# Kernel tuning notes

Hardware: AMD Instinct MI355X
Metric: run time of the kernel (lower is better)

Reference implementation:

```python
import jax, jax.numpy as jnp
import numpy as np

B, S, E, H = 8, 2048, 384, 6
D = E // H  # head dim = 64


def setup_inputs() -> dict:
    key = jax.random.key(0)
    ks = jax.random.split(key, 5)
    s = 1.0 / np.sqrt(E)
    return {
        "x": jax.random.normal(ks[0], (B, S, E), dtype=jnp.float32),
        "Wq": jax.random.normal(ks[1], (E, E), dtype=jnp.float32) * s,
        "Wk": jax.random.normal(ks[2], (E, E), dtype=jnp.float32) * s,
        "Wv": jax.random.normal(ks[3], (E, E), dtype=jnp.float32) * s,
        "Wo": jax.random.normal(ks[4], (E, E), dtype=jnp.float32) * s,
        "bo": jnp.zeros((E,), dtype=jnp.float32),
    }


def reference(x, Wq, Wk, Wv, Wo, bo):
    b, s, e = x.shape
    # QKV projections (torch Linear with bias=False: x @ W.T; here W stored as [in,out])
    q = (x @ Wq).reshape(b, s, H, D).transpose(0, 2, 1, 3)  # [b,h,s,d]
    k = (x @ Wk).reshape(b, s, H, D).transpose(0, 2, 1, 3)
    v = (x @ Wv).reshape(b, s, H, D).transpose(0, 2, 1, 3)
    scores = jnp.einsum("bhqd,bhkd->bhqk", q, k) / jnp.sqrt(jnp.asarray(D, x.dtype))
    causal = jnp.tril(jnp.ones((s, s), dtype=bool))
    scores = jnp.where(causal, scores, -jnp.inf)
    attn = jax.nn.softmax(scores, axis=-1)
    # NOTE: original applies dropout but then uses the PRE-dropout softmax for @V,
    # so dropout is a no-op; we faithfully omit it.
    out = jnp.einsum("bhqk,bhkd->bhqd", attn, v)  # [b,h,s,d]
    out = out.transpose(0, 2, 1, 3).reshape(b, s, e)
    return out @ Wo + bo
```

## Files before the change

kernel.cpp:

```cpp
#include <hip/hip_runtime.h>
#include <hip/hip_bf16.h>
#include <cstdint>
#include <cstddef>

typedef __attribute__((ext_vector_type(8))) short short8;
typedef __attribute__((ext_vector_type(4))) float f32x4;

#define S_LEN 2048
#define EMB 384
#define NH 6
#define HD 64
#define NB 8
#define QSCALE 0.180336880f

__device__ __forceinline__ unsigned short f2bf(float f) {
  unsigned u = __builtin_bit_cast(unsigned, f);
  u += 0x7fffu + ((u >> 16) & 1u);
  return (unsigned short)(u >> 16);
}

__global__ __launch_bounds__(256) void k_prep(
    const float* __restrict__ x, unsigned short* __restrict__ xb,
    const float* __restrict__ Wq, const float* __restrict__ Wk,
    const float* __restrict__ Wv, const float* __restrict__ Wo,
    unsigned short* __restrict__ Wqt, unsigned short* __restrict__ Wkt,
    unsigned short* __restrict__ Wvt, unsigned short* __restrict__ Wot) {
  const int tid = threadIdx.x;
  if (blockIdx.x < 1536) {
    int i = blockIdx.x * 256 + tid;
    const int n4 = (NB * S_LEN * EMB) / 4;
    for (; i < n4; i += 1536 * 256) {
      const float4 v = reinterpret_cast<const float4*>(x)[i];
      ushort4 o;
      o.x = f2bf(v.x); o.y = f2bf(v.y); o.z = f2bf(v.z); o.w = f2bf(v.w);
      reinterpret_cast<ushort4*>(xb)[i] = o;
    }
  } else {
    const int idx = (blockIdx.x - 1536) * 256 + tid;
    const int mat = idx / 147456;
    const int rem = idx - mat * 147456;
    const int k = rem / 384;
    const int n = rem - k * 384;
    const float* W = (mat == 0) ? Wq : (mat == 1) ? Wk : (mat == 2) ? Wv : Wo;
    unsigned short* Wt = (mat == 0) ? Wqt : (mat == 1) ? Wkt : (mat == 2) ? Wvt : Wot;
    Wt[n * 384 + k] = f2bf(W[rem]);
  }
}

__global__ __launch_bounds__(256) void k_qkv(
    const unsigned short* __restrict__ xb,
    const unsigned short* __restrict__ Wqt,
    const unsigned short* __restrict__ Wkt,
    const unsigned short* __restrict__ Wvt,
    unsigned short* __restrict__ Qb,
    unsigned short* __restrict__ Kb,
    unsigned short* __restrict__ Vb) {
  __shared__ __attribute__((aligned(16))) unsigned short La[128 * 72];

  const int tid = threadIdx.x;
  const int lane = tid & 63;
  const int w = tid >> 6;
  const int wr = w >> 1, wc = w & 1;
  const int lr = lane & 15, lg = lane >> 4;
  const int m0 = blockIdx.x * 128;
  const int wsel = blockIdx.y / 3;
  const int n0 = (blockIdx.y % 3) * 128;
  const unsigned short* Wt = (wsel == 0) ? Wqt : (wsel == 1) ? Wkt : Wvt;
  unsigned short* Out = (wsel == 0) ? Qb : (wsel == 1) ? Kb : Vb;

  const int srow = tid >> 3;
  const int sg = tid & 7;

  f32x4 acc[4][4] = {};
  short8 st[4];
#pragma unroll
  for (int i = 0; i < 4; ++i)
    st[i] = *reinterpret_cast<const short8*>(
        xb + (size_t)(m0 + i * 32 + srow) * EMB + sg * 8);

  for (int kt = 0; kt < 6; ++kt) {
    __syncthreads();
#pragma unroll
    for (int i = 0; i < 4; ++i)
      *reinterpret_cast<short8*>(&La[(i * 32 + srow) * 72 + sg * 8]) = st[i];
    __syncthreads();
    if (kt < 5) {
      const int kn = (kt + 1) * 64;
#pragma unroll
      for (int i = 0; i < 4; ++i)
        st[i] = *reinterpret_cast<const short8*>(
            xb + (size_t)(m0 + i * 32 + srow) * EMB + kn + sg * 8);
    }
#pragma unroll
    for (int kk = 0; kk < 2; ++kk) {
      short8 a[4], b[4];
#pragma unroll
      for (int ms = 0; ms < 4; ++ms)
        a[ms] = *reinterpret_cast<const short8*>(
            &La[(wr * 64 + ms * 16 + lr) * 72 + kk * 32 + lg * 8]);
#pragma unroll
      for (int ns = 0; ns < 4; ++ns)
        b[ns] = *reinterpret_cast<const short8*>(
            Wt + (size_t)(n0 + wc * 64 + ns * 16 + lr) * EMB + kt * 64 + kk * 32 + lg * 8);
#pragma unroll
      for (int ms = 0; ms < 4; ++ms)
#pragma unroll
        for (int ns = 0; ns < 4; ++ns)
          acc[ms][ns] = __builtin_amdgcn_mfma_f32_16x16x32_bf16(
              a[ms], b[ns], acc[ms][ns], 0, 0, 0);
    }
  }

  const float sc = (wsel == 0) ? QSCALE : 1.0f;
#pragma unroll
  for (int ms = 0; ms < 4; ++ms)
#pragma unroll
    for (int ns = 0; ns < 4; ++ns)
#pragma unroll
      for (int r = 0; r < 4; ++r) {
        const int m = m0 + wr * 64 + ms * 16 + lg * 4 + r;
        const int n = n0 + wc * 64 + ns * 16 + lr;
        const int bb = m >> 11;
        const int s = m & 2047;
        const int h = n >> 6;
        const int d = n & 63;
        Out[(((size_t)bb * NH + h) * S_LEN + s) * HD + d] = f2bf(acc[ms][ns][r] * sc);
      }
}

__global__ __launch_bounds__(256) void k_vt(const unsigned short* __restrict__ Vb,
                                            unsigned short* __restrict__ Vtg) {
  __shared__ unsigned short L[64 * 65];
  const int tid = threadIdx.x;
  const int g = tid & 7;
  const int h = tid >> 3;
  const int st = blockIdx.x;
  const int bh = blockIdx.y;
  const unsigned short* src = Vb + (size_t)bh * S_LEN * HD + (size_t)st * 64 * HD;
  unsigned short* dst = Vtg + (size_t)bh * S_LEN * HD;

#pragma unroll
  for (int c = 0; c < 2; ++c) {
    const int s = h + 32 * c;
    const short8 v = *reinterpret_cast<const short8*>(src + s * HD + g * 8);
#pragma unroll
    for (int j = 0; j < 8; ++j) L[s * 65 + g * 8 + j] = (unsigned short)v[j];
  }
  __syncthreads();
#pragma unroll
  for (int c = 0; c < 2; ++c) {
    const int d = h + 32 * c;
    short8 v;
#pragma unroll
    for (int j = 0; j < 8; ++j) v[j] = (short)L[(g * 8 + j) * 65 + d];
    *reinterpret_cast<short8*>(dst + (size_t)d * S_LEN + st * 64 + g * 8) = v;
  }
}

__global__ __launch_bounds__(256) void k_attn(
    const unsigned short* __restrict__ Qb,
    const unsigned short* __restrict__ Kb,
    const unsigned short* __restrict__ Vtg,
    unsigned short* __restrict__ Ob) {
  __shared__ __attribute__((aligned(16))) unsigned short Ks[64 * 64];
  __shared__ __attribute__((aligned(16))) unsigned short Vt[64 * 64];
  __shared__ __attribute__((aligned(16))) unsigned short Ps[64 * 64];

  const int tid = threadIdx.x;
  const int lane = tid & 63;
  const int w = tid >> 6;
  const int lr = lane & 15, lg = lane >> 4;

  const int lin = blockIdx.y * 16 + blockIdx.x;
  const int swz = (lin & 7) * 96 + (lin >> 3);
  const int pair = swz & 15;
  const int bh = swz >> 4;

  const unsigned short* Qp = Qb + (size_t)bh * S_LEN * HD;
  const unsigned short* Kp = Kb + (size_t)bh * S_LEN * HD;
  const unsigned short* Vp = Vtg + (size_t)bh * S_LEN * HD;
  const int b = bh / NH, hh = bh - b * NH;

  const int srow = tid >> 3;
  const int sslot = tid & 7;
  const int wsl0 = (sslot ^ (srow & 7)) << 3;

  for (int phase = 0; phase < 2; ++phase) {
    const int qt = phase ? (31 - pair) : pair;
    const int qbase = qt * 64 + w * 16;

    const short8 aq0 = *reinterpret_cast<const short8*>(Qp + (size_t)(qbase + lr) * HD + lg * 8);
    const short8 aq1 = *reinterpret_cast<const short8*>(Qp + (size_t)(qbase + lr) * HD + 32 + lg * 8);

    f32x4 o[4] = {};
    float l_i[4] = {0.f, 0.f, 0.f, 0.f};

    short8 pk0 = *reinterpret_cast<const short8*>(Kp + (size_t)srow * HD + sslot * 8);
    short8 pk1 = *reinterpret_cast<const short8*>(Kp + (size_t)(srow + 32) * HD + sslot * 8);
    short8 pv0 = *reinterpret_cast<const short8*>(Vp + (size_t)srow * S_LEN + sslot * 8);
    short8 pv1 = *reinterpret_cast<const short8*>(Vp + (size_t)(srow + 32) * S_LEN + sslot * 8);

    for (int t = 0; t <= qt; ++t) {
      __syncthreads();
      *reinterpret_cast<short8*>(&Ks[srow * 64 + wsl0]) = pk0;
      *reinterpret_cast<short8*>(&Ks[(srow + 32) * 64 + wsl0]) = pk1;
      *reinterpret_cast<short8*>(&Vt[srow * 64 + wsl0]) = pv0;
      *reinterpret_cast<short8*>(&Vt[(srow + 32) * 64 + wsl0]) = pv1;
      __syncthreads();

      if (t < qt) {
        const int tn = (t + 1) * 64;
        pk0 = *reinterpret_cast<const short8*>(Kp + (size_t)(tn + srow) * HD + sslot * 8);
        pk1 = *reinterpret_cast<const short8*>(Kp + (size_t)(tn + srow + 32) * HD + sslot * 8);
        pv0 = *reinterpret_cast<const short8*>(Vp + (size_t)srow * S_LEN + tn + sslot * 8);
        pv1 = *reinterpret_cast<const short8*>(Vp + (size_t)(srow + 32) * S_LEN + tn + sslot * 8);
      }

      float sv[4][4];
#pragma unroll
      for (int ks = 0; ks < 4; ++ks) {
        const int kstart = t * 64 + ks * 16;
        if (kstart > qbase + 15) {
#pragma unroll
          for (int r = 0; r < 4; ++r) sv[ks][r] = -1e30f;
        } else {
          const int krow = ks * 16 + lr;
          const int kx = krow & 7;
          const short8 bk0 = *reinterpret_cast<const short8*>(&Ks[krow * 64 + ((lg ^ kx) << 3)]);
          const short8 bk1 = *reinterpret_cast<const short8*>(&Ks[krow * 64 + (((4 + lg) ^ kx) << 3)]);
          f32x4 s = {};
          s = __builtin_amdgcn_mfma_f32_16x16x32_bf16(aq0, bk0, s, 0, 0, 0);
          s = __builtin_amdgcn_mfma_f32_16x16x32_bf16(aq1, bk1, s, 0, 0, 0);
          if (kstart + 15 <= qbase) {
#pragma unroll
            for (int r = 0; r < 4; ++r) sv[ks][r] = s[r];
          } else {
            const int kg = kstart + lr;
#pragma unroll
            for (int r = 0; r < 4; ++r)
              sv[ks][r] = (kg <= qbase + lg * 4 + r) ? s[r] : -1e30f;
          }
        }
      }

#pragma unroll
      for (int r = 0; r < 4; ++r) {
        const int q = w * 16 + lg * 4 + r;
        const int qx = q & 7;
        const int abase = q * 64 + (lr & 7);
        const int sp = lr >> 3;
        float p[4];
#pragma unroll
        for (int ks = 0; ks < 4; ++ks) p[ks] = __builtin_amdgcn_exp2f(sv[ks][r]);
        l_i[r] += (p[0] + p[1]) + (p[2] + p[3]);
#pragma unroll
        for (int ks = 0; ks < 4; ++ks)
          Ps[abase + ((((ks << 1) | sp) ^ qx) << 3)] = f2bf(p[ks]);
      }

      const int qrow = w * 16 + lr;
      const int qx2 = qrow & 7;
#pragma unroll
      for (int kk = 0; kk < 2; ++kk) {
        const short8 ap = *reinterpret_cast<const short8*>(
            &Ps[qrow * 64 + (((kk * 4 + lg) ^ qx2) << 3)]);
#pragma unroll
        for (int ns = 0; ns < 4; ++ns) {
          const int vrow = ns * 16 + lr;
          const short8 bv = *reinterpret_cast<const short8*>(
              &Vt[vrow * 64 + (((kk * 4 + lg) ^ (vrow & 7)) << 3)]);
          o[ns] = __builtin_amdgcn_mfma_f32_16x16x32_bf16(ap, bv, o[ns], 0, 0, 0);
        }
      }
    }

#pragma unroll
    for (int r = 0; r < 4; ++r) {
      float l = l_i[r];
      l += __shfl_xor(l, 1);
      l += __shfl_xor(l, 2);
      l += __shfl_xor(l, 4);
      l += __shfl_xor(l, 8);
      l_i[r] = 1.0f / l;
    }
#pragma unroll
    for (int ns = 0; ns < 4; ++ns)
#pragma unroll
      for (int r = 0; r < 4; ++r) {
        const int qg = qbase + lg * 4 + r;
        const float val = o[ns][r] * l_i[r];
        Ob[((size_t)(b * S_LEN + qg)) * EMB + hh * HD + ns * 16 + lr] = f2bf(val);
      }
  }
}

__global__ __launch_bounds__(256) void k_oproj(
    const unsigned short* __restrict__ Ob,
    const unsigned short* __restrict__ Wot,
    const float* __restrict__ bo,
    float* __restrict__ out) {
  __shared__ __attribute__((aligned(16))) unsigned short La[128 * 72];

  const int tid = threadIdx.x;
  const int lane = tid & 63;
  const int w = tid >> 6;
  const int wr = w >> 1, wc = w & 1;
  const int lr = lane & 15, lg = lane >> 4;
  const int m0 = blockIdx.x * 128;
  const int n0 = blockIdx.y * 128;

  const int srow = tid >> 3;
  const int sg = tid & 7;

  f32x4 acc[4][4] = {};
  short8 st[4];
#pragma unroll
  for (int i = 0; i < 4; ++i)
    st[i] = *reinterpret_cast<const short8*>(
        Ob + (size_t)(m0 + i * 32 + srow) * EMB + sg * 8);

  for (int kt = 0; kt < 6; ++kt) {
    __syncthreads();
#pragma unroll
    for (int i = 0; i < 4; ++i)
      *reinterpret_cast<short8*>(&La[(i * 32 + srow) * 72 + sg * 8]) = st[i];
    __syncthreads();
    if (kt < 5) {
      const int kn = (kt + 1) * 64;
#pragma unroll
      for (int i = 0; i < 4; ++i)
        st[i] = *reinterpret_cast<const short8*>(
            Ob + (size_t)(m0 + i * 32 + srow) * EMB + kn + sg * 8);
    }
#pragma unroll
    for (int kk = 0; kk < 2; ++kk) {
      short8 a[4], b[4];
#pragma unroll
      for (int ms = 0; ms < 4; ++ms)
        a[ms] = *reinterpret_cast<const short8*>(
            &La[(wr * 64 + ms * 16 + lr) * 72 + kk * 32 + lg * 8]);
#pragma unroll
      for (int ns = 0; ns < 4; ++ns)
        b[ns] = *reinterpret_cast<const short8*>(
            Wot + (size_t)(n0 + wc * 64 + ns * 16 + lr) * EMB + kt * 64 + kk * 32 + lg * 8);
#pragma unroll
      for (int ms = 0; ms < 4; ++ms)
#pragma unroll
        for (int ns = 0; ns < 4; ++ns)
          acc[ms][ns] = __builtin_amdgcn_mfma_f32_16x16x32_bf16(
              a[ms], b[ns], acc[ms][ns], 0, 0, 0);
    }
  }

#pragma unroll
  for (int ms = 0; ms < 4; ++ms)
#pragma unroll
    for (int ns = 0; ns < 4; ++ns)
#pragma unroll
      for (int r = 0; r < 4; ++r) {
        const int m = m0 + wr * 64 + ms * 16 + lg * 4 + r;
        const int n = n0 + wc * 64 + ns * 16 + lr;
        out[(size_t)m * EMB + n] = acc[ms][ns][r] + bo[n];
      }
}

extern "C" void kernel_launch(void* const* d_in, const int* in_sizes, int n_in,
                              void* d_out, int out_size, void* d_ws, size_t ws_size,
                              hipStream_t stream) {
  const float* x  = (const float*)d_in[0];
  const float* Wq = (const float*)d_in[1];
  const float* Wk = (const float*)d_in[2];
  const float* Wv = (const float*)d_in[3];
  const float* Wo = (const float*)d_in[4];
  const float* bo = (const float*)d_in[5];
  float* out = (float*)d_out;

  uint8_t* ws = (uint8_t*)d_ws;
  unsigned short* xb  = (unsigned short*)(ws);
  unsigned short* Wqt = (unsigned short*)(ws + 12582912);
  unsigned short* Wkt = (unsigned short*)(ws + 12877824);
  unsigned short* Wvt = (unsigned short*)(ws + 13172736);
  unsigned short* Wot = (unsigned short*)(ws + 13467648);
  unsigned short* Qb  = (unsigned short*)(ws + 13762560);
  unsigned short* Kb  = (unsigned short*)(ws + 26345472);
  unsigned short* Vb  = (unsigned short*)(ws + 38928384);
  unsigned short* Ob  = (unsigned short*)(ws + 51511296);
  unsigned short* VT  = xb;

  hipLaunchKernelGGL(k_prep, dim3(3840), dim3(256), 0, stream,
                     x, xb, Wq, Wk, Wv, Wo, Wqt, Wkt, Wvt, Wot);
  hipLaunchKernelGGL(k_qkv, dim3(128, 9), dim3(256), 0, stream,
                     xb, Wqt, Wkt, Wvt, Qb, Kb, Vb);
  hipLaunchKernelGGL(k_vt, dim3(S_LEN / 64, NB * NH), dim3(256), 0, stream, Vb, VT);
  hipLaunchKernelGGL(k_attn, dim3(16, 48), dim3(256), 0, stream, Qb, Kb, VT, Ob);
  hipLaunchKernelGGL(k_oproj, dim3(128, 3), dim3(256), 0, stream, Ob, Wot, bo, out);
}
```

Baseline: 215.5 us.

## Fuse V transpose into QKV GEMM, tile weight transpose, split attention blocks

The V transpose moves into the QKV GEMM epilogue through an LDS swizzled tile, which removes the separate k_vt kernel and a round trip of V through global memory. The weight conversion in prep now uses LDS-tiled transposes instead of scattered scalar writes. Attention now launches one block per query tile, longest tiles first, instead of pairing tiles inside a block, and adds s_setprio around the MFMA sections. The GEMMs register double-buffer the B operand. The changes add code complexity and register pressure.

```diff
diff --git a/kernel.cpp b/kernel.cpp
--- a/kernel.cpp
+++ b/kernel.cpp
@@ -14,9 +14,7 @@
 #define QSCALE 0.180336880f
 
 __device__ __forceinline__ unsigned short f2bf(float f) {
-  unsigned u = __builtin_bit_cast(unsigned, f);
-  u += 0x7fffu + ((u >> 16) & 1u);
-  return (unsigned short)(u >> 16);
+  return __builtin_bit_cast(unsigned short, __float2bfloat16(f));
 }
 
 __global__ __launch_bounds__(256) void k_prep(
@@ -36,14 +34,34 @@
       reinterpret_cast<ushort4*>(xb)[i] = o;
     }
   } else {
-    const int idx = (blockIdx.x - 1536) * 256 + tid;
-    const int mat = idx / 147456;
-    const int rem = idx - mat * 147456;
-    const int k = rem / 384;
-    const int n = rem - k * 384;
+    __shared__ unsigned short Lw[64 * 66];
+    const int bx2 = blockIdx.x - 1536;
+    const int mat = bx2 / 36;
+    const int tile = bx2 - mat * 36;
+    const int k0 = (tile / 6) * 64;
+    const int n0 = (tile % 6) * 64;
     const float* W = (mat == 0) ? Wq : (mat == 1) ? Wk : (mat == 2) ? Wv : Wo;
     unsigned short* Wt = (mat == 0) ? Wqt : (mat == 1) ? Wkt : (mat == 2) ? Wvt : Wot;
-    Wt[n * 384 + k] = f2bf(W[rem]);
+    const int f4 = tid & 15;
+#pragma unroll
+    for (int it = 0; it < 4; ++it) {
+      const int kl = it * 16 + (tid >> 4);
+      const float4 v = reinterpret_cast<const float4*>(W + (size_t)(k0 + kl) * EMB + n0)[f4];
+      Lw[kl * 66 + f4 * 4 + 0] = f2bf(v.x);
+      Lw[kl * 66 + f4 * 4 + 1] = f2bf(v.y);
+      Lw[kl * 66 + f4 * 4 + 2] = f2bf(v.z);
+      Lw[kl * 66 + f4 * 4 + 3] = f2bf(v.w);
+    }
+    __syncthreads();
+    const int g = tid & 7;
+#pragma unroll
+    for (int it = 0; it < 2; ++it) {
+      const int nl = it * 32 + (tid >> 3);
+      short8 o;
+#pragma unroll
+      for (int j = 0; j < 8; ++j) o[j] = (short)Lw[(g * 8 + j) * 66 + nl];
+      *reinterpret_cast<short8*>(Wt + (size_t)(n0 + nl) * EMB + k0 + g * 8) = o;
+    }
   }
 }
 
@@ -54,8 +72,9 @@
     const unsigned short* __restrict__ Wvt,
     unsigned short* __restrict__ Qb,
     unsigned short* __restrict__ Kb,
-    unsigned short* __restrict__ Vb) {
+    unsigned short* __restrict__ Vtb) {
   __shared__ __attribute__((aligned(16))) unsigned short La[128 * 72];
+  __shared__ __attribute__((aligned(16))) unsigned short Lt[64 * 136];
 
   const int tid = threadIdx.x;
   const int lane = tid & 63;
@@ -66,19 +85,28 @@
   const int wsel = blockIdx.y / 3;
   const int n0 = (blockIdx.y % 3) * 128;
   const unsigned short* Wt = (wsel == 0) ? Wqt : (wsel == 1) ? Wkt : Wvt;
-  unsigned short* Out = (wsel == 0) ? Qb : (wsel == 1) ? Kb : Vb;
 
   const int srow = tid >> 3;
   const int sg = tid & 7;
 
   f32x4 acc[4][4] = {};
   short8 st[4];
+  short8 breg[2][2][4];
+
 #pragma unroll
   for (int i = 0; i < 4; ++i)
     st[i] = *reinterpret_cast<const short8*>(
         xb + (size_t)(m0 + i * 32 + srow) * EMB + sg * 8);
-
+#pragma unroll
+  for (int kk = 0; kk < 2; ++kk)
+#pragma unroll
+    for (int ns = 0; ns < 4; ++ns)
+      breg[0][kk][ns] = *reinterpret_cast<const short8*>(
+          Wt + (size_t)(n0 + wc * 64 + ns * 16 + lr) * EMB + kk * 32 + lg * 8);
+
+#pragma unroll
   for (int kt = 0; kt < 6; ++kt) {
+    const int cur = kt & 1, nxt = cur ^ 1;
     __syncthreads();
 #pragma unroll
     for (int i = 0; i < 4; ++i)
@@ -90,70 +118,76 @@
       for (int i = 0; i < 4; ++i)
         st[i] = *reinterpret_cast<const short8*>(
             xb + (size_t)(m0 + i * 32 + srow) * EMB + kn + sg * 8);
+#pragma unroll
+      for (int kk = 0; kk < 2; ++kk)
+#pragma unroll
+        for (int ns = 0; ns < 4; ++ns)
+          breg[nxt][kk][ns] = *reinterpret_cast<const short8*>(
+              Wt + (size_t)(n0 + wc * 64 + ns * 16 + lr) * EMB + kn + kk * 32 + lg * 8);
     }
 #pragma unroll
     for (int kk = 0; kk < 2; ++kk) {
-      short8 a[4], b[4];
+      short8 a[4];
 #pragma unroll
       for (int ms = 0; ms < 4; ++ms)
         a[ms] = *reinterpret_cast<const short8*>(
             &La[(wr * 64 + ms * 16 + lr) * 72 + kk * 32 + lg * 8]);
 #pragma unroll
-      for (int ns = 0; ns < 4; ++ns)
-        b[ns] = *reinterpret_cast<const short8*>(
-            Wt + (size_t)(n0 + wc * 64 + ns * 16 + lr) * EMB + kt * 64 + kk * 32 + lg * 8);
-#pragma unroll
       for (int ms = 0; ms < 4; ++ms)
 #pragma unroll
         for (int ns = 0; ns < 4; ++ns)
           acc[ms][ns] = __builtin_amdgcn_mfma_f32_16x16x32_bf16(
-              a[ms], b[ns], acc[ms][ns], 0, 0, 0);
-    }
-  }
-
-  const float sc = (wsel == 0) ? QSCALE : 1.0f;
-#pragma unroll
-  for (int ms = 0; ms < 4; ++ms)
-#pragma unroll
-    for (int ns = 0; ns < 4; ++ns)
-#pragma unroll
-      for (int r = 0; r < 4; ++r) {
-        const int m = m0 + wr * 64 + ms * 16 + lg * 4 + r;
-        const int n = n0 + wc * 64 + ns * 16 + lr;
-        const int bb = m >> 11;
-        const int s = m & 2047;
-        const int h = n >> 6;
-        const int d = n & 63;
-        Out[(((size_t)bb * NH + h) * S_LEN + s) * HD + d] = f2bf(acc[ms][ns][r] * sc);
+              a[ms], breg[cur][kk][ns], acc[ms][ns], 0, 0, 0);
+    }
+  }
+
+  if (wsel != 2) {
+    unsigned short* Out = (wsel == 0) ? Qb : Kb;
+    const float sc = (wsel == 0) ? QSCALE : 1.0f;
+#pragma unroll
+    for (int ms = 0; ms < 4; ++ms)
+#pragma unroll
+      for (int ns = 0; ns < 4; ++ns)
+#pragma unroll
+        for (int r = 0; r < 4; ++r) {
+          const int m = m0 + wr * 64 + ms * 16 + lg * 4 + r;
+          const int n = n0 + wc * 64 + ns * 16 + lr;
+          const int bb = m >> 11;
+          const int s = m & 2047;
+          const int h = n >> 6;
+          const int d = n & 63;
+          Out[(((size_t)bb * NH + h) * S_LEN + s) * HD + d] = f2bf(acc[ms][ns][r] * sc);
+        }
+  } else {
+    const int bb = m0 >> 11;
+    const int s0 = m0 & 2047;
+#pragma unroll
+    for (int p = 0; p < 2; ++p) {
+      __syncthreads();
+      if (wc == p) {
+#pragma unroll
+        for (int ms = 0; ms < 4; ++ms)
+#pragma unroll
+          for (int ns = 0; ns < 4; ++ns)
+#pragma unroll
+            for (int r = 0; r < 4; ++r) {
+              const int dl = ns * 16 + lr;
+              const int ml = wr * 64 + ms * 16 + lg * 4 + r;
+              Lt[dl * 136 + (((ml >> 3) ^ (dl & 7)) << 3) + (ml & 7)] = f2bf(acc[ms][ns][r]);
+            }
       }
-}
-
-__global__ __launch_bounds__(256) void k_vt(const unsigned short* __restrict__ Vb,
-                                            unsigned short* __restrict__ Vtg) {
-  __shared__ unsigned short L[64 * 65];
-  const int tid = threadIdx.x;
-  const int g = tid & 7;
-  const int h = tid >> 3;
-  const int st = blockIdx.x;
-  const int bh = blockIdx.y;
-  const unsigned short* src = Vb + (size_t)bh * S_LEN * HD + (size_t)st * 64 * HD;
-  unsigned short* dst = Vtg + (size_t)bh * S_LEN * HD;
-
-#pragma unroll
-  for (int c = 0; c < 2; ++c) {
-    const int s = h + 32 * c;
-    const short8 v = *reinterpret_cast<const short8*>(src + s * HD + g * 8);
-#pragma unroll
-    for (int j = 0; j < 8; ++j) L[s * 65 + g * 8 + j] = (unsigned short)v[j];
-  }
-  __syncthreads();
-#pragma unroll
-  for (int c = 0; c < 2; ++c) {
-    const int d = h + 32 * c;
-    short8 v;
-#pragma unroll
-    for (int j = 0; j < 8; ++j) v[j] = (short)L[(g * 8 + j) * 65 + d];
-    *reinterpret_cast<short8*>(dst + (size_t)d * S_LEN + st * 64 + g * 8) = v;
+      __syncthreads();
+      const int hg = 2 * (blockIdx.y % 3) + p;
+      const int c = tid & 15;
+#pragma unroll
+      for (int it = 0; it < 4; ++it) {
+        const int d = it * 16 + (tid >> 4);
+        const short8 v = *reinterpret_cast<const short8*>(
+            &Lt[d * 136 + ((c ^ (d & 7)) << 3)]);
+        *reinterpret_cast<short8*>(
+            Vtb + (((size_t)bb * NH + hg) * HD + d) * S_LEN + s0 + c * 8) = v;
+      }
+    }
   }
 }
 
@@ -171,10 +205,10 @@
   const int w = tid >> 6;
   const int lr = lane & 15, lg = lane >> 4;
 
-  const int lin = blockIdx.y * 16 + blockIdx.x;
-  const int swz = (lin & 7) * 96 + (lin >> 3);
-  const int pair = swz & 15;
-  const int bh = swz >> 4;
+  const int lin = blockIdx.x;
+  const int idx = lin >> 3;
+  const int bh = (lin & 7) * 6 + (idx >> 5);
+  const int qt = 31 - (idx & 31);
 
   const unsigned short* Qp = Qb + (size_t)bh * S_LEN * HD;
   const unsigned short* Kp = Kb + (size_t)bh * S_LEN * HD;
@@ -185,113 +219,114 @@
   const int sslot = tid & 7;
   const int wsl0 = (sslot ^ (srow & 7)) << 3;
 
-  for (int phase = 0; phase < 2; ++phase) {
-    const int qt = phase ? (31 - pair) : pair;
-    const int qbase = qt * 64 + w * 16;
-
-    const short8 aq0 = *reinterpret_cast<const short8*>(Qp + (size_t)(qbase + lr) * HD + lg * 8);
-    const short8 aq1 = *reinterpret_cast<const short8*>(Qp + (size_t)(qbase + lr) * HD + 32 + lg * 8);
-
-    f32x4 o[4] = {};
-    float l_i[4] = {0.f, 0.f, 0.f, 0.f};
-
-    short8 pk0 = *reinterpret_cast<const short8*>(Kp + (size_t)srow * HD + sslot * 8);
-    short8 pk1 = *reinterpret_cast<const short8*>(Kp + (size_t)(srow + 32) * HD + sslot * 8);
-    short8 pv0 = *reinterpret_cast<const short8*>(Vp + (size_t)srow * S_LEN + sslot * 8);
-    short8 pv1 = *reinterpret_cast<const short8*>(Vp + (size_t)(srow + 32) * S_LEN + sslot * 8);
-
-    for (int t = 0; t <= qt; ++t) {
-      __syncthreads();
-      *reinterpret_cast<short8*>(&Ks[srow * 64 + wsl0]) = pk0;
-      *reinterpret_cast<short8*>(&Ks[(srow + 32) * 64 + wsl0]) = pk1;
-      *reinterpret_cast<short8*>(&Vt[srow * 64 + wsl0]) = pv0;
-      *reinterpret_cast<short8*>(&Vt[(srow + 32) * 64 + wsl0]) = pv1;
-      __syncthreads();
-
-      if (t < qt) {
-        const int tn = (t + 1) * 64;
-        pk0 = *reinterpret_cast<const short8*>(Kp + (size_t)(tn + srow) * HD + sslot * 8);
-        pk1 = *reinterpret_cast<const short8*>(Kp + (size_t)(tn + srow + 32) * HD + sslot * 8);
-        pv0 = *reinterpret_cast<const short8*>(Vp + (size_t)srow * S_LEN + tn + sslot * 8);
-        pv1 = *reinterpret_cast<const short8*>(Vp + (size_t)(srow + 32) * S_LEN + tn + sslot * 8);
-      }
-
-      float sv[4][4];
-#pragma unroll
-      for (int ks = 0; ks < 4; ++ks) {
-        const int kstart = t * 64 + ks * 16;
-        if (kstart > qbase + 15) {
-#pragma unroll
-          for (int r = 0; r < 4; ++r) sv[ks][r] = -1e30f;
+  const int qbase = qt * 64 + w * 16;
+
+  const short8 aq0 = *reinterpret_cast<const short8*>(Qp + (size_t)(qbase + lr) * HD + lg * 8);
+  const short8 aq1 = *reinterpret_cast<const short8*>(Qp + (size_t)(qbase + lr) * HD + 32 + lg * 8);
+
+  f32x4 o[4] = {};
+  float l_i[4] = {0.f, 0.f, 0.f, 0.f};
+
+  short8 pk0 = *reinterpret_cast<const short8*>(Kp + (size_t)srow * HD + sslot * 8);
+  short8 pk1 = *reinterpret_cast<const short8*>(Kp + (size_t)(srow + 32) * HD + sslot * 8);
+  short8 pv0 = *reinterpret_cast<const short8*>(Vp + (size_t)srow * S_LEN + sslot * 8);
+  short8 pv1 = *reinterpret_cast<const short8*>(Vp + (size_t)(srow + 32) * S_LEN + sslot * 8);
+
+  for (int t = 0; t <= qt; ++t) {
+    __syncthreads();
+    *reinterpret_cast<short8*>(&Ks[srow * 64 + wsl0]) = pk0;
+    *reinterpret_cast<short8*>(&Ks[(srow + 32) * 64 + wsl0]) = pk1;
+    *reinterpret_cast<short8*>(&Vt[srow * 64 + wsl0]) = pv0;
+    *reinterpret_cast<short8*>(&Vt[(srow + 32) * 64 + wsl0]) = pv1;
+    __syncthreads();
+
+    if (t < qt) {
+      const int tn = (t + 1) * 64;
+      pk0 = *reinterpret_cast<const short8*>(Kp + (size_t)(tn + srow) * HD + sslot * 8);
+      pk1 = *reinterpret_cast<const short8*>(Kp + (size_t)(tn + srow + 32) * HD + sslot * 8);
+      pv0 = *reinterpret_cast<const short8*>(Vp + (size_t)srow * S_LEN + tn + sslot * 8);
+      pv1 = *reinterpret_cast<const short8*>(Vp + (size_t)(srow + 32) * S_LEN + tn + sslot * 8);
+    }
+
+    float sv[4][4];
+    __builtin_amdgcn_s_setprio(1);
+#pragma unroll
+    for (int ks = 0; ks < 4; ++ks) {
+      const int kstart = t * 64 + ks * 16;
+      if (kstart > qbase + 15) {
+#pragma unroll
+        for (int r = 0; r < 4; ++r) sv[ks][r] = -1e30f;
+      } else {
+        const int krow = ks * 16 + lr;
+        const int kx = krow & 7;
+        const short8 bk0 = *reinterpret_cast<const short8*>(&Ks[krow * 64 + ((lg ^ kx) << 3)]);
+        const short8 bk1 = *reinterpret_cast<const short8*>(&Ks[krow * 64 + (((4 + lg) ^ kx) << 3)]);
+        f32x4 s = {};
+        s = __builtin_amdgcn_mfma_f32_16x16x32_bf16(aq0, bk0, s, 0, 0, 0);
+        s = __builtin_amdgcn_mfma_f32_16x16x32_bf16(aq1, bk1, s, 0, 0, 0);
+        if (kstart + 15 <= qbase) {
+#pragma unroll
+          for (int r = 0; r < 4; ++r) sv[ks][r] = s[r];
         } else {
-          const int krow = ks * 16 + lr;
-          const int kx = krow & 7;
-          const short8 bk0 = *reinterpret_cast<const short8*>(&Ks[krow * 64 + ((lg ^ kx) << 3)]);
-          const short8 bk1 = *reinterpret_cast<const short8*>(&Ks[krow * 64 + (((4 + lg) ^ kx) << 3)]);
-          f32x4 s = {};
-          s = __builtin_amdgcn_mfma_f32_16x16x32_bf16(aq0, bk0, s, 0, 0, 0);
-          s = __builtin_amdgcn_mfma_f32_16x16x32_bf16(aq1, bk1, s, 0, 0, 0);
-          if (kstart + 15 <= qbase) {
-#pragma unroll
-            for (int r = 0; r < 4; ++r) sv[ks][r] = s[r];
-          } else {
-            const int kg = kstart + lr;
-#pragma unroll
-            for (int r = 0; r < 4; ++r)
-              sv[ks][r] = (kg <= qbase + lg * 4 + r) ? s[r] : -1e30f;
-          }
+          const int kg = kstart + lr;
+#pragma unroll
+          for (int r = 0; r < 4; ++r)
+            sv[ks][r] = (kg <= qbase + lg * 4 + r) ? s[r] : -1e30f;
         }
       }
-
-#pragma unroll
-      for (int r = 0; r < 4; ++r) {
-        const int q = w * 16 + lg * 4 + r;
-        const int qx = q & 7;
-        const int abase = q * 64 + (lr & 7);
-        const int sp = lr >> 3;
-        float p[4];
-#pragma unroll
-        for (int ks = 0; ks < 4; ++ks) p[ks] = __builtin_amdgcn_exp2f(sv[ks][r]);
-        l_i[r] += (p[0] + p[1]) + (p[2] + p[3]);
-#pragma unroll
-        for (int ks = 0; ks < 4; ++ks)
-          Ps[abase + ((((ks << 1) | sp) ^ qx) << 3)] = f2bf(p[ks]);
+    }
+    __builtin_amdgcn_s_setprio(0);
+
+#pragma unroll
+    for (int r = 0; r < 4; ++r) {
+      const int q = w * 16 + lg * 4 + r;
+      const int qx = q & 7;
+      const int abase = q * 64 + (lr & 7);
+      const int sp = lr >> 3;
+      float p[4];
+#pragma unroll
+      for (int ks = 0; ks < 4; ++ks) p[ks] = __builtin_amdgcn_exp2f(sv[ks][r]);
+      l_i[r] += (p[0] + p[1]) + (p[2] + p[3]);
+#pragma unroll
+      for (int ks = 0; ks < 4; ++ks)
+        Ps[abase + ((((ks << 1) | sp) ^ qx) << 3)] = f2bf(p[ks]);
+    }
+
+    const int qrow = w * 16 + lr;
+    const int qx2 = qrow & 7;
+    __builtin_amdgcn_s_setprio(1);
+#pragma unroll
+    for (int kk = 0; kk < 2; ++kk) {
+      const short8 ap = *reinterpret_cast<const short8*>(
+          &Ps[qrow * 64 + (((kk * 4 + lg) ^ qx2) << 3)]);
+#pragma unroll
+      for (int ns = 0; ns < 4; ++ns) {
+        const int vrow = ns * 16 + lr;
+        const short8 bv = *reinterpret_cast<const short8*>(
+            &Vt[vrow * 64 + (((kk * 4 + lg) ^ (vrow & 7)) << 3)]);
+        o[ns] = __builtin_amdgcn_mfma_f32_16x16x32_bf16(ap, bv, o[ns], 0, 0, 0);
       }
-
-      const int qrow = w * 16 + lr;
-      const int qx2 = qrow & 7;
-#pragma unroll
-      for (int kk = 0; kk < 2; ++kk) {
-        const short8 ap = *reinterpret_cast<const short8*>(
-            &Ps[qrow * 64 + (((kk * 4 + lg) ^ qx2) << 3)]);
-#pragma unroll
-        for (int ns = 0; ns < 4; ++ns) {
-          const int vrow = ns * 16 + lr;
-          const short8 bv = *reinterpret_cast<const short8*>(
-              &Vt[vrow * 64 + (((kk * 4 + lg) ^ (vrow & 7)) << 3)]);
-          o[ns] = __builtin_amdgcn_mfma_f32_16x16x32_bf16(ap, bv, o[ns], 0, 0, 0);
-        }
-      }
-    }
-
+    }
+    __builtin_amdgcn_s_setprio(0);
+  }
+
+#pragma unroll
+  for (int r = 0; r < 4; ++r) {
+    float l = l_i[r];
+    l += __shfl_xor(l, 1);
+    l += __shfl_xor(l, 2);
+    l += __shfl_xor(l, 4);
+    l += __shfl_xor(l, 8);
+    l_i[r] = 1.0f / l;
+  }
+#pragma unroll
+  for (int ns = 0; ns < 4; ++ns)
 #pragma unroll
     for (int r = 0; r < 4; ++r) {
-      float l = l_i[r];
-      l += __shfl_xor(l, 1);
-      l += __shfl_xor(l, 2);
-      l += __shfl_xor(l, 4);
-      l += __shfl_xor(l, 8);
-      l_i[r] = 1.0f / l;
-    }
-#pragma unroll
-    for (int ns = 0; ns < 4; ++ns)
-#pragma unroll
-      for (int r = 0; r < 4; ++r) {
-        const int qg = qbase + lg * 4 + r;
-        const float val = o[ns][r] * l_i[r];
-        Ob[((size_t)(b * S_LEN + qg)) * EMB + hh * HD + ns * 16 + lr] = f2bf(val);
-      }
-  }
+      const int qg = qbase + lg * 4 + r;
+      const float val = o[ns][r] * l_i[r];
+      Ob[((size_t)(b * S_LEN + qg)) * EMB + hh * HD + ns * 16 + lr] = f2bf(val);
+    }
 }
 
 __global__ __launch_bounds__(256) void k_oproj(
@@ -314,12 +349,22 @@
 
   f32x4 acc[4][4] = {};
   short8 st[4];
+  short8 breg[2][2][4];
+
 #pragma unroll
   for (int i = 0; i < 4; ++i)
     st[i] = *reinterpret_cast<const short8*>(
         Ob + (size_t)(m0 + i * 32 + srow) * EMB + sg * 8);
-
+#pragma unroll
+  for (int kk = 0; kk < 2; ++kk)
+#pragma unroll
+    for (int ns = 0; ns < 4; ++ns)
+      breg[0][kk][ns] = *reinterpret_cast<const short8*>(
+          Wot + (size_t)(n0 + wc * 64 + ns * 16 + lr) * EMB + kk * 32 + lg * 8);
+
+#pragma unroll
   for (int kt = 0; kt < 6; ++kt) {
+    const int cur = kt & 1, nxt = cur ^ 1;
     __syncthreads();
 #pragma unroll
     for (int i = 0; i < 4; ++i)
@@ -331,24 +376,26 @@
       for (int i = 0; i < 4; ++i)
         st[i] = *reinterpret_cast<const short8*>(
             Ob + (size_t)(m0 + i * 32 + srow) * EMB + kn + sg * 8);
+#pragma unroll
+      for (int kk = 0; kk < 2; ++kk)
+#pragma unroll
+        for (int ns = 0; ns < 4; ++ns)
+          breg[nxt][kk][ns] = *reinterpret_cast<const short8*>(
+              Wot + (size_t)(n0 + wc * 64 + ns * 16 + lr) * EMB + kn + kk * 32 + lg * 8);
     }
 #pragma unroll
     for (int kk = 0; kk < 2; ++kk) {
-      short8 a[4], b[4];
+      short8 a[4];
 #pragma unroll
       for (int ms = 0; ms < 4; ++ms)
         a[ms] = *reinterpret_cast<const short8*>(
             &La[(wr * 64 + ms * 16 + lr) * 72 + kk * 32 + lg * 8]);
 #pragma unroll
-      for (int ns = 0; ns < 4; ++ns)
-        b[ns] = *reinterpret_cast<const short8*>(
-            Wot + (size_t)(n0 + wc * 64 + ns * 16 + lr) * EMB + kt * 64 + kk * 32 + lg * 8);
-#pragma unroll
       for (int ms = 0; ms < 4; ++ms)
 #pragma unroll
         for (int ns = 0; ns < 4; ++ns)
           acc[ms][ns] = __builtin_amdgcn_mfma_f32_16x16x32_bf16(
-              a[ms], b[ns], acc[ms][ns], 0, 0, 0);
+              a[ms], breg[cur][kk][ns], acc[ms][ns], 0, 0, 0);
     }
   }
 
@@ -383,15 +430,13 @@
   unsigned short* Wot = (unsigned short*)(ws + 13467648);
   unsigned short* Qb  = (unsigned short*)(ws + 13762560);
   unsigned short* Kb  = (unsigned short*)(ws + 26345472);
-  unsigned short* Vb  = (unsigned short*)(ws + 38928384);
+  unsigned short* VT  = (unsigned short*)(ws + 38928384);
   unsigned short* Ob  = (unsigned short*)(ws + 51511296);
-  unsigned short* VT  = xb;
-
-  hipLaunchKernelGGL(k_prep, dim3(3840), dim3(256), 0, stream,
+
+  hipLaunchKernelGGL(k_prep, dim3(1680), dim3(256), 0, stream,
                      x, xb, Wq, Wk, Wv, Wo, Wqt, Wkt, Wvt, Wot);
   hipLaunchKernelGGL(k_qkv, dim3(128, 9), dim3(256), 0, stream,
-                     xb, Wqt, Wkt, Wvt, Qb, Kb, Vb);
-  hipLaunchKernelGGL(k_vt, dim3(S_LEN / 64, NB * NH), dim3(256), 0, stream, Vb, VT);
-  hipLaunchKernelGGL(k_attn, dim3(16, 48), dim3(256), 0, stream, Qb, Kb, VT, Ob);
+                     xb, Wqt, Wkt, Wvt, Qb, Kb, VT);
+  hipLaunchKernelGGL(k_attn, dim3(1536), dim3(256), 0, stream, Qb, Kb, VT, Ob);
   hipLaunchKernelGGL(k_oproj, dim3(128, 3), dim3(256), 0, stream, Ob, Wot, bo, out);
 }
```

After: 201.8 us. 1.07x faster.
